# Performance work log

Measured on AMD Instinct MI355X. Metric: run time of the kernel, lower is better.

Reference implementation:

```python
import jax, jax.numpy as jnp
import numpy as np

N = 100_000      # nodes
E = 3_200_000    # edges (avg degree 32)
F_IN = 64        # num_node_features
G = 256          # graphs in batch


def _lin(key, fan_in, fan_out):
    kw, kb = jax.random.split(key)
    bound = 1.0 / np.sqrt(fan_in)
    W = jax.random.uniform(kw, (fan_in, fan_out), jnp.float32, -bound, bound)
    b = jax.random.uniform(kb, (fan_out,), jnp.float32, -bound, bound)
    return W, b


def setup_inputs() -> dict:
    key = jax.random.key(0)
    ks = jax.random.split(key, 9)
    x = jax.random.normal(ks[0], (N, F_IN), jnp.float32)
    edge_index = jax.random.randint(ks[1], (2, E), 0, N, dtype=jnp.int64)
    batch = jnp.sort(jax.random.randint(ks[2], (N,), 0, G, dtype=jnp.int64))
    W1, b1 = _lin(ks[3], F_IN, 60)
    W2, b2 = _lin(ks[4], 60, 50)
    Wf1, bf1 = _lin(ks[5], 50, 30)
    Wf2, bf2 = _lin(ks[6], 30, 20)
    Wf3, bf3 = _lin(ks[7], 20, 10)
    Wo, bo = _lin(ks[8], 10, 1)
    return {"x": x, "edge_index": edge_index, "batch": batch,
            "W1": W1, "b1": b1, "W2": W2, "b2": b2,
            "Wf1": Wf1, "bf1": bf1, "Wf2": Wf2, "bf2": bf2,
            "Wf3": Wf3, "bf3": bf3, "Wo": Wo, "bo": bo}


def _gcn_norm(edge_index, n_nodes):
    # add self loops, then symmetric D^{-1/2} (A+I) D^{-1/2} edge weights
    loop = jnp.arange(n_nodes, dtype=edge_index.dtype)
    src = jnp.concatenate([edge_index[0], loop])
    dst = jnp.concatenate([edge_index[1], loop])
    deg = jax.ops.segment_sum(jnp.ones_like(dst, dtype=jnp.float32), dst,
                              num_segments=n_nodes)
    dinv = jax.lax.rsqrt(deg)  # deg >= 1 thanks to self loops
    norm = dinv[src] * dinv[dst]
    return src, dst, norm


def _gcn_conv(h, W, b, src, dst, norm, n_nodes):
    h = h @ W                                            # [N, out]
    msg = h[src] * norm[:, None]                         # gather over edges
    agg = jax.ops.segment_sum(msg, dst, num_segments=n_nodes)
    return agg + b


def reference(x, edge_index, batch, W1, b1, W2, b2,
              Wf1, bf1, Wf2, bf2, Wf3, bf3, Wo, bo):
    n_nodes = x.shape[0]
    src, dst, norm = _gcn_norm(edge_index, n_nodes)
    h = _gcn_conv(x, W1, b1, src, dst, norm, n_nodes)    # [N, 60]
    h = _gcn_conv(h, W2, b2, src, dst, norm, n_nodes)    # [N, 50]
    # global_add_pool over graph ids
    g = jax.ops.segment_sum(h, batch, num_segments=G)    # [G, 50]
    # MLP stack (no nonlinearities in the original forward)
    g = g @ Wf1 + bf1
    g = g @ Wf2 + bf2
    g = g @ Wf3 + bf3
    return g @ Wo + bo                                   # [G, 1]
```

## Files before the change

### kernel.cpp

```cpp
#include <hip/hip_runtime.h>


#define RSHIFT 7
#define RNODES 128
#define NB_MAX 1024
#define NBLK 512
#define STHREADS 512
#define STAGE_CAP 8192
#define BCAP 6144

__global__ void collapse_weights_k(
    const float* __restrict__ W1, const float* __restrict__ b1,
    const float* __restrict__ W2, const float* __restrict__ b2,
    const float* __restrict__ Wf1, const float* __restrict__ bf1,
    const float* __restrict__ Wf2, const float* __restrict__ bf2,
    const float* __restrict__ Wf3, const float* __restrict__ bf3,
    const float* __restrict__ Wo, const float* __restrict__ bo,
    float* __restrict__ w1c, float* __restrict__ sc,
    int* __restrict__ cursor)
{
    __shared__ float wo[10], w3[20], w2[30], w1[50], w2c[60];
    const int t = threadIdx.x;
    for (int b = t; b < NB_MAX; b += 64) cursor[b] = 0;
    if (t < 10) wo[t] = Wo[t];
    __syncthreads();
    if (t < 20) { float s = 0.f; for (int j = 0; j < 10; ++j) s += Wf3[t*10+j]*wo[j]; w3[t] = s; }
    __syncthreads();
    if (t < 30) { float s = 0.f; for (int j = 0; j < 20; ++j) s += Wf2[t*20+j]*w3[j]; w2[t] = s; }
    __syncthreads();
    if (t < 50) { float s = 0.f; for (int j = 0; j < 30; ++j) s += Wf1[t*30+j]*w2[j]; w1[t] = s; }
    __syncthreads();
    if (t < 60) { float s = 0.f; for (int j = 0; j < 50; ++j) s += W2[t*50+j]*w1[j]; w2c[t] = s; }
    __syncthreads();
    { float s = 0.f; for (int j = 0; j < 60; ++j) s += W1[t*60+j]*w2c[j]; w1c[t] = s; }
    if (t == 0) {
        float c1 = 0.f; for (int j = 0; j < 60; ++j) c1 += b1[j]*w2c[j];
        float c2 = 0.f; for (int j = 0; j < 50; ++j) c2 += b2[j]*w1[j];
        float c0 = bo[0];
        for (int j = 0; j < 30; ++j) c0 += bf1[j]*w2[j];
        for (int j = 0; j < 20; ++j) c0 += bf2[j]*w3[j];
        for (int j = 0; j < 10; ++j) c0 += bf3[j]*wo[j];
        sc[0] = c1; sc[1] = c2; sc[2] = c0;
    }
}

__global__ void node_u_k(const float* __restrict__ x, const float* __restrict__ w1c,
                         float* __restrict__ u,
                         const float* __restrict__ sc, float* __restrict__ out,
                         int n, int G) {
    int tid = blockIdx.x * blockDim.x + threadIdx.x;
    if (tid < G) out[tid] = sc[2];
    int wave = tid >> 6;
    int lane = threadIdx.x & 63;
    int node = wave * 4 + (lane >> 4);
    int sub = lane & 15;
    if (node >= n) return;
    float4 xv = *reinterpret_cast<const float4*>(x + (size_t)node * 64 + sub * 4);
    float4 wv = *reinterpret_cast<const float4*>(w1c + sub * 4);
    float val = xv.x * wv.x + xv.y * wv.y + xv.z * wv.z + xv.w * wv.w;
    val += __shfl_down(val, 8, 16);
    val += __shfl_down(val, 4, 16);
    val += __shfl_down(val, 2, 16);
    val += __shfl_down(val, 1, 16);
    if (sub == 0) u[node] = val;
}

__global__ void scatter_k(const int* __restrict__ src, const int* __restrict__ dst,
                          int E, int chunk, int nb,
                          int* __restrict__ cursor,
                          unsigned int* __restrict__ binned) {
    __shared__ int hist[NB_MAX];
    __shared__ int tbase[NB_MAX];
    __shared__ int adj[NB_MAX];
    __shared__ int sums[STHREADS];
    __shared__ unsigned int staged[STAGE_CAP];
    __shared__ unsigned short bof[STAGE_CAP];
    const int tid = threadIdx.x;
    hist[tid] = 0; hist[tid + 512] = 0;
    __syncthreads();
    int e0 = blockIdx.x * chunk;
    int e1 = e0 + chunk; if (e1 > E) e1 = E;
    const int QMAX = STAGE_CAP / (STHREADS * 4);
    unsigned int pk[QMAX * 4];
    int bk[QMAX * 4];
    int rk[QMAX * 4];
    int nv[QMAX];
    #pragma unroll
    for (int j = 0; j < QMAX; ++j) {
        int i = e0 + tid * 4 + j * (STHREADS * 4);
        int cnt = e1 - i; if (cnt > 4) cnt = 4; if (cnt < 0) cnt = 0;
        nv[j] = cnt;
        if (cnt == 4) {
            int4 s4 = *reinterpret_cast<const int4*>(src + i);
            int4 d4 = *reinterpret_cast<const int4*>(dst + i);
            pk[j*4+0] = (unsigned)s4.x | ((unsigned)(d4.x & (RNODES-1)) << 17);
            pk[j*4+1] = (unsigned)s4.y | ((unsigned)(d4.y & (RNODES-1)) << 17);
            pk[j*4+2] = (unsigned)s4.z | ((unsigned)(d4.z & (RNODES-1)) << 17);
            pk[j*4+3] = (unsigned)s4.w | ((unsigned)(d4.w & (RNODES-1)) << 17);
            bk[j*4+0] = d4.x >> RSHIFT; bk[j*4+1] = d4.y >> RSHIFT;
            bk[j*4+2] = d4.z >> RSHIFT; bk[j*4+3] = d4.w >> RSHIFT;
            rk[j*4+0] = atomicAdd(&hist[bk[j*4+0]], 1);
            rk[j*4+1] = atomicAdd(&hist[bk[j*4+1]], 1);
            rk[j*4+2] = atomicAdd(&hist[bk[j*4+2]], 1);
            rk[j*4+3] = atomicAdd(&hist[bk[j*4+3]], 1);
        } else {
            for (int l = 0; l < cnt; ++l) {
                int s = src[i + l], d = dst[i + l];
                pk[j*4+l] = (unsigned)s | ((unsigned)(d & (RNODES-1)) << 17);
                bk[j*4+l] = d >> RSHIFT;
                rk[j*4+l] = atomicAdd(&hist[bk[j*4+l]], 1);
            }
        }
    }
    __syncthreads();
    int h0 = hist[2*tid], h1 = hist[2*tid+1];
    int pair = h0 + h1;
    sums[tid] = pair;
    __syncthreads();
    for (int off = 1; off < STHREADS; off <<= 1) {
        int a = (tid >= off) ? sums[tid - off] : 0;
        __syncthreads();
        sums[tid] += a;
        __syncthreads();
    }
    int excl = sums[tid] - pair;
    tbase[2*tid] = excl;
    tbase[2*tid+1] = excl + h0;
    {
        int b0 = 2*tid, b1 = 2*tid + 1;
        if (b0 < nb && h0 > 0) {
            int r = atomicAdd(&cursor[b0], h0);
            adj[b0] = b0 * BCAP + r - excl;
        }
        if (b1 < nb && h1 > 0) {
            int r = atomicAdd(&cursor[b1], h1);
            adj[b1] = b1 * BCAP + r - (excl + h0);
        }
    }
    __syncthreads();
    #pragma unroll
    for (int j = 0; j < QMAX; ++j) {
        for (int l = 0; l < nv[j]; ++l) {
            int b = bk[j*4+l];
            int slot = tbase[b] + rk[j*4+l];
            staged[slot] = pk[j*4+l];
            bof[slot] = (unsigned short)b;
        }
    }
    __syncthreads();
    int tcount = e1 - e0;
    for (int s = tid; s < tcount; s += STHREADS) {
        int b = bof[s];
        binned[adj[b] + s] = staged[s];
    }
}

__global__ void degree_dinv_k(const unsigned int* __restrict__ binned,
                              const int* __restrict__ cursor,
                              const float* __restrict__ u,
                              float* __restrict__ dinv, float* __restrict__ w, int n) {
    __shared__ int cnt[RNODES];
    int tid = threadIdx.x, b = blockIdx.x;
    if (tid < RNODES) cnt[tid] = 0;
    __syncthreads();
    int s0 = b * BCAP;
    int c = cursor[b];
    int nvec = c >> 2;
    for (int k = tid; k < nvec; k += blockDim.x) {
        uint4 p = *reinterpret_cast<const uint4*>(binned + s0 + 4 * k);
        atomicAdd(&cnt[p.x >> 17], 1);
        atomicAdd(&cnt[p.y >> 17], 1);
        atomicAdd(&cnt[p.z >> 17], 1);
        atomicAdd(&cnt[p.w >> 17], 1);
    }
    int i = 4 * nvec + tid;
    if (i < c) atomicAdd(&cnt[binned[s0 + i] >> 17], 1);
    __syncthreads();
    int g = (b << RSHIFT) + tid;
    if (tid < RNODES && g < n) {
        float d = rsqrtf((float)(cnt[tid] + 1));
        dinv[g] = d;
        w[g] = d * u[g];
    }
}

__global__ void conv_mid_k(const unsigned int* __restrict__ binned,
                           const int* __restrict__ cursor,
                           const float* __restrict__ w, const float* __restrict__ dinv,
                           const float* __restrict__ u, const float* __restrict__ sc,
                           float* __restrict__ v, float* __restrict__ wb, int n) {
    __shared__ float acc[RNODES];
    int tid = threadIdx.x, b = blockIdx.x;
    if (tid < RNODES) acc[tid] = 0.f;
    __syncthreads();
    int s0 = b * BCAP;
    int cnt = cursor[b];
    int nvec = cnt >> 2;
    for (int k = tid; k < nvec; k += blockDim.x) {
        uint4 p = *reinterpret_cast<const uint4*>(binned + s0 + 4 * k);
        float wx = w[p.x & 0x1FFFF];
        float wy = w[p.y & 0x1FFFF];
        float wz = w[p.z & 0x1FFFF];
        float ww = w[p.w & 0x1FFFF];
        atomicAdd(&acc[p.x >> 17], wx);
        atomicAdd(&acc[p.y >> 17], wy);
        atomicAdd(&acc[p.z >> 17], wz);
        atomicAdd(&acc[p.w >> 17], ww);
    }
    int i = 4 * nvec + tid;
    if (i < cnt) { unsigned p = binned[s0 + i]; atomicAdd(&acc[p >> 17], w[p & 0x1FFFF]); }
    __syncthreads();
    int g = (b << RSHIFT) + tid;
    if (tid < RNODES && g < n) {
        float di = dinv[g];
        float val = sc[0] + di * acc[tid] + di * di * u[g];
        v[g] = val;
        wb[g] = di * val;
    }
}

__global__ void conv_final_k(const unsigned int* __restrict__ binned,
                             const int* __restrict__ cursor,
                             const float* __restrict__ wb, const float* __restrict__ dinv,
                             const float* __restrict__ v, const float* __restrict__ sc,
                             const int* __restrict__ batch, float* __restrict__ out, int n) {
    __shared__ float acc[RNODES];
    __shared__ float tbuf[RNODES];
    __shared__ int gbuf[RNODES];
    int tid = threadIdx.x, b = blockIdx.x;
    if (tid < RNODES) acc[tid] = 0.f;
    __syncthreads();
    int s0 = b * BCAP;
    int cnt = cursor[b];
    int nvec = cnt >> 2;
    for (int k = tid; k < nvec; k += blockDim.x) {
        uint4 p = *reinterpret_cast<const uint4*>(binned + s0 + 4 * k);
        float wx = wb[p.x & 0x1FFFF];
        float wy = wb[p.y & 0x1FFFF];
        float wz = wb[p.z & 0x1FFFF];
        float ww = wb[p.w & 0x1FFFF];
        atomicAdd(&acc[p.x >> 17], wx);
        atomicAdd(&acc[p.y >> 17], wy);
        atomicAdd(&acc[p.z >> 17], wz);
        atomicAdd(&acc[p.w >> 17], ww);
    }
    int i = 4 * nvec + tid;
    if (i < cnt) { unsigned p = binned[s0 + i]; atomicAdd(&acc[p >> 17], wb[p & 0x1FFFF]); }
    __syncthreads();
    int g = (b << RSHIFT) + tid;
    float tval = 0.f; int gid = -1;
    if (tid < RNODES && g < n) {
        float di = dinv[g];
        tval = sc[1] + di * acc[tid] + di * di * v[g];
        gid = batch[g];
    }
    if (tid < RNODES) { tbuf[tid] = tval; gbuf[tid] = gid; }
    __syncthreads();
    if (tid < RNODES && g < n) {
        bool head = (tid == 0) || (gbuf[tid - 1] != gid);
        if (head) {
            float s = 0.f;
            int i2 = tid;
            while (i2 < RNODES && gbuf[i2] == gid) { s += tbuf[i2]; ++i2; }
            atomicAdd(&out[gid], s);
        }
    }
}

extern "C" void kernel_launch(void* const* d_in, const int* in_sizes, int n_in,
                              void* d_out, int out_size, void* d_ws, size_t ws_size,
                              hipStream_t stream)
{
    const float* x    = (const float*)d_in[0];
    const int*   ei   = (const int*)d_in[1];
    const int*   batch= (const int*)d_in[2];
    const float* W1   = (const float*)d_in[3];
    const float* b1   = (const float*)d_in[4];
    const float* W2   = (const float*)d_in[5];
    const float* b2   = (const float*)d_in[6];
    const float* Wf1  = (const float*)d_in[7];
    const float* bf1  = (const float*)d_in[8];
    const float* Wf2  = (const float*)d_in[9];
    const float* bf2  = (const float*)d_in[10];
    const float* Wf3  = (const float*)d_in[11];
    const float* bf3  = (const float*)d_in[12];
    const float* Wo   = (const float*)d_in[13];
    const float* bo   = (const float*)d_in[14];
    float* out = (float*)d_out;

    const int n = in_sizes[0] / 64;
    const int E = in_sizes[1] / 2;
    const int G = out_size;
    const int* src = ei;
    const int* dst = ei + E;
    const int nb = (n + RNODES - 1) >> RSHIFT;

    float* ws_f = (float*)d_ws;
    int*   ws_i = (int*)d_ws;
    float* w1c    = ws_f;
    float* sc     = ws_f + 64;
    int*   cursor = ws_i + 128;
    size_t off_u  = 128 + (size_t)NB_MAX;
    float* u      = ws_f + off_u;
    float* dinv   = u + n;
    float* w      = dinv + n;
    float* v      = w + n;
    float* wb     = v + n;
    size_t off_b  = off_u + 5*(size_t)n;
    off_b = (off_b + 3) & ~(size_t)3;
    unsigned int* binned = (unsigned int*)(ws_f + off_b);

    int chunk = (E + NBLK - 1) / NBLK;
    chunk = (chunk + 3) & ~3;

    hipLaunchKernelGGL(collapse_weights_k, dim3(1), dim3(64), 0, stream,
                       W1, b1, W2, b2, Wf1, bf1, Wf2, bf2, Wf3, bf3, Wo, bo,
                       w1c, sc, cursor);
    hipLaunchKernelGGL(node_u_k, dim3((n / 4 * 64 + 255) / 256 + 1), dim3(256), 0, stream,
                       x, w1c, u, sc, out, n, G);
    hipLaunchKernelGGL(scatter_k, dim3(NBLK), dim3(STHREADS), 0, stream,
                       src, dst, E, chunk, nb, cursor, binned);
    hipLaunchKernelGGL(degree_dinv_k, dim3(nb), dim3(512), 0, stream,
                       binned, cursor, u, dinv, w, n);
    hipLaunchKernelGGL(conv_mid_k, dim3(nb), dim3(512), 0, stream,
                       binned, cursor, w, dinv, u, sc, v, wb, n);
    hipLaunchKernelGGL(conv_final_k, dim3(nb), dim3(512), 0, stream,
                       binned, cursor, wb, dinv, v, sc, batch, out, n);
}
```

Baseline: 210.5 us.

## Fuse node projection into scatter kernel and move output init to collapse kernel

Removes the separate node_u_k launch. Each scatter block now first computes the per-node dot product u for its slice of nodes, then does edge binning. Output initialisation moves into the single-block weight-collapse kernel. The change also adds launch bounds, unrolls the tail loops, and clamps bin counts to BCAP. It saves one kernel launch and its tail, but the scatter blocks now run serial extra work before binning starts, which could lengthen the critical path.

```diff
diff --git a/kernel.cpp b/kernel.cpp
--- a/kernel.cpp
+++ b/kernel.cpp
@@ -4,8 +4,8 @@
 #define RSHIFT 7
 #define RNODES 128
 #define NB_MAX 1024
-#define NBLK 512
-#define STHREADS 512
+#define GRID 512
+#define THREADS 512
 #define STAGE_CAP 8192
 #define BCAP 6144
 
@@ -17,9 +17,10 @@
     const float* __restrict__ Wf3, const float* __restrict__ bf3,
     const float* __restrict__ Wo, const float* __restrict__ bo,
     float* __restrict__ w1c, float* __restrict__ sc,
-    int* __restrict__ cursor)
+    int* __restrict__ cursor, float* __restrict__ out, int G)
 {
     __shared__ float wo[10], w3[20], w2[30], w1[50], w2c[60];
+    __shared__ float c0s;
     const int t = threadIdx.x;
     for (int b = t; b < NB_MAX; b += 64) cursor[b] = 0;
     if (t < 10) wo[t] = Wo[t];
@@ -41,53 +42,61 @@
         for (int j = 0; j < 20; ++j) c0 += bf2[j]*w3[j];
         for (int j = 0; j < 10; ++j) c0 += bf3[j]*wo[j];
         sc[0] = c1; sc[1] = c2; sc[2] = c0;
-    }
-}
-
-__global__ void node_u_k(const float* __restrict__ x, const float* __restrict__ w1c,
-                         float* __restrict__ u,
-                         const float* __restrict__ sc, float* __restrict__ out,
-                         int n, int G) {
-    int tid = blockIdx.x * blockDim.x + threadIdx.x;
-    if (tid < G) out[tid] = sc[2];
-    int wave = tid >> 6;
-    int lane = threadIdx.x & 63;
-    int node = wave * 4 + (lane >> 4);
-    int sub = lane & 15;
-    if (node >= n) return;
-    float4 xv = *reinterpret_cast<const float4*>(x + (size_t)node * 64 + sub * 4);
-    float4 wv = *reinterpret_cast<const float4*>(w1c + sub * 4);
-    float val = xv.x * wv.x + xv.y * wv.y + xv.z * wv.z + xv.w * wv.w;
-    val += __shfl_down(val, 8, 16);
-    val += __shfl_down(val, 4, 16);
-    val += __shfl_down(val, 2, 16);
-    val += __shfl_down(val, 1, 16);
-    if (sub == 0) u[node] = val;
-}
-
-__global__ void scatter_k(const int* __restrict__ src, const int* __restrict__ dst,
-                          int E, int chunk, int nb,
-                          int* __restrict__ cursor,
-                          unsigned int* __restrict__ binned) {
+        c0s = c0;
+    }
+    __syncthreads();
+    for (int g = t; g < G; g += 64) out[g] = c0s;
+}
+
+__global__ __launch_bounds__(THREADS, 4)
+void scatter_u_k(const float* __restrict__ x, const float* __restrict__ w1c,
+                 float* __restrict__ u,
+                 const int* __restrict__ src, const int* __restrict__ dst,
+                 int E, int n, int npb, int chunk, int nb,
+                 int* __restrict__ cursor, unsigned int* __restrict__ binned) {
     __shared__ int hist[NB_MAX];
     __shared__ int tbase[NB_MAX];
     __shared__ int adj[NB_MAX];
-    __shared__ int sums[STHREADS];
+    __shared__ int sums[THREADS];
     __shared__ unsigned int staged[STAGE_CAP];
     __shared__ unsigned short bof[STAGE_CAP];
     const int tid = threadIdx.x;
-    hist[tid] = 0; hist[tid + 512] = 0;
-    __syncthreads();
-    int e0 = blockIdx.x * chunk;
+    const int bx = blockIdx.x;
+
+    {
+        const int grp = tid >> 4, sub = tid & 15;
+        float4 wv = *reinterpret_cast<const float4*>(w1c + sub * 4);
+        int base = bx * npb;
+        for (int p = 0; p * 32 < npb; ++p) {
+            int nl = p * 32 + grp;
+            int g = base + nl;
+            bool ok = (nl < npb) && (g < n);
+            float val = 0.f;
+            if (ok) {
+                float4 xv = *reinterpret_cast<const float4*>(
+                    x + (size_t)g * 64 + sub * 4);
+                val = xv.x*wv.x + xv.y*wv.y + xv.z*wv.z + xv.w*wv.w;
+            }
+            val += __shfl_down(val, 8, 16);
+            val += __shfl_down(val, 4, 16);
+            val += __shfl_down(val, 2, 16);
+            val += __shfl_down(val, 1, 16);
+            if (ok && sub == 0) u[g] = val;
+        }
+    }
+
+    hist[tid] = 0; hist[tid + THREADS] = 0;
+    __syncthreads();
+    int e0 = bx * chunk;
     int e1 = e0 + chunk; if (e1 > E) e1 = E;
-    const int QMAX = STAGE_CAP / (STHREADS * 4);
+    const int QMAX = STAGE_CAP / (THREADS * 4);
     unsigned int pk[QMAX * 4];
     int bk[QMAX * 4];
     int rk[QMAX * 4];
     int nv[QMAX];
     #pragma unroll
     for (int j = 0; j < QMAX; ++j) {
-        int i = e0 + tid * 4 + j * (STHREADS * 4);
+        int i = e0 + tid * 4 + j * (THREADS * 4);
         int cnt = e1 - i; if (cnt > 4) cnt = 4; if (cnt < 0) cnt = 0;
         nv[j] = cnt;
         if (cnt == 4) {
@@ -104,11 +113,14 @@
             rk[j*4+2] = atomicAdd(&hist[bk[j*4+2]], 1);
             rk[j*4+3] = atomicAdd(&hist[bk[j*4+3]], 1);
         } else {
-            for (int l = 0; l < cnt; ++l) {
-                int s = src[i + l], d = dst[i + l];
-                pk[j*4+l] = (unsigned)s | ((unsigned)(d & (RNODES-1)) << 17);
-                bk[j*4+l] = d >> RSHIFT;
-                rk[j*4+l] = atomicAdd(&hist[bk[j*4+l]], 1);
+            #pragma unroll
+            for (int l = 0; l < 4; ++l) {
+                if (l < cnt) {
+                    int s = src[i + l], d = dst[i + l];
+                    pk[j*4+l] = (unsigned)s | ((unsigned)(d & (RNODES-1)) << 17);
+                    bk[j*4+l] = d >> RSHIFT;
+                    rk[j*4+l] = atomicAdd(&hist[bk[j*4+l]], 1);
+                }
             }
         }
     }
@@ -117,7 +129,7 @@
     int pair = h0 + h1;
     sums[tid] = pair;
     __syncthreads();
-    for (int off = 1; off < STHREADS; off <<= 1) {
+    for (int off = 1; off < THREADS; off <<= 1) {
         int a = (tid >= off) ? sums[tid - off] : 0;
         __syncthreads();
         sums[tid] += a;
@@ -140,16 +152,19 @@
     __syncthreads();
     #pragma unroll
     for (int j = 0; j < QMAX; ++j) {
-        for (int l = 0; l < nv[j]; ++l) {
-            int b = bk[j*4+l];
-            int slot = tbase[b] + rk[j*4+l];
-            staged[slot] = pk[j*4+l];
-            bof[slot] = (unsigned short)b;
+        #pragma unroll
+        for (int l = 0; l < 4; ++l) {
+            if (l < nv[j]) {
+                int b = bk[j*4+l];
+                int slot = tbase[b] + rk[j*4+l];
+                staged[slot] = pk[j*4+l];
+                bof[slot] = (unsigned short)b;
+            }
         }
     }
     __syncthreads();
     int tcount = e1 - e0;
-    for (int s = tid; s < tcount; s += STHREADS) {
+    for (int s = tid; s < tcount; s += THREADS) {
         int b = bof[s];
         binned[adj[b] + s] = staged[s];
     }
@@ -165,6 +180,7 @@
     __syncthreads();
     int s0 = b * BCAP;
     int c = cursor[b];
+    if (c > BCAP) c = BCAP;
     int nvec = c >> 2;
     for (int k = tid; k < nvec; k += blockDim.x) {
         uint4 p = *reinterpret_cast<const uint4*>(binned + s0 + 4 * k);
@@ -195,6 +211,7 @@
     __syncthreads();
     int s0 = b * BCAP;
     int cnt = cursor[b];
+    if (cnt > BCAP) cnt = BCAP;
     int nvec = cnt >> 2;
     for (int k = tid; k < nvec; k += blockDim.x) {
         uint4 p = *reinterpret_cast<const uint4*>(binned + s0 + 4 * k);
@@ -232,6 +249,7 @@
     __syncthreads();
     int s0 = b * BCAP;
     int cnt = cursor[b];
+    if (cnt > BCAP) cnt = BCAP;
     int nvec = cnt >> 2;
     for (int k = tid; k < nvec; k += blockDim.x) {
         uint4 p = *reinterpret_cast<const uint4*>(binned + s0 + 4 * k);
@@ -310,16 +328,15 @@
     off_b = (off_b + 3) & ~(size_t)3;
     unsigned int* binned = (unsigned int*)(ws_f + off_b);
 
-    int chunk = (E + NBLK - 1) / NBLK;
+    int chunk = (E + GRID - 1) / GRID;
     chunk = (chunk + 3) & ~3;
+    int npb = (n + GRID - 1) / GRID;
 
     hipLaunchKernelGGL(collapse_weights_k, dim3(1), dim3(64), 0, stream,
                        W1, b1, W2, b2, Wf1, bf1, Wf2, bf2, Wf3, bf3, Wo, bo,
-                       w1c, sc, cursor);
-    hipLaunchKernelGGL(node_u_k, dim3((n / 4 * 64 + 255) / 256 + 1), dim3(256), 0, stream,
-                       x, w1c, u, sc, out, n, G);
-    hipLaunchKernelGGL(scatter_k, dim3(NBLK), dim3(STHREADS), 0, stream,
-                       src, dst, E, chunk, nb, cursor, binned);
+                       w1c, sc, cursor, out, G);
+    hipLaunchKernelGGL(scatter_u_k, dim3(GRID), dim3(THREADS), 0, stream,
+                       x, w1c, u, src, dst, E, n, npb, chunk, nb, cursor, binned);
     hipLaunchKernelGGL(degree_dinv_k, dim3(nb), dim3(512), 0, stream,
                        binned, cursor, u, dinv, w, n);
     hipLaunchKernelGGL(conv_mid_k, dim3(nb), dim3(512), 0, stream,
```

Measured after the change: 203.1 us. 3.5% less time.
